# Kernel optimization log

Measured on AMD Instinct MI355X. Metric: run time of the kernel, lower is better.

## Reference

```python
import jax, jax.numpy as jnp
import numpy as np

ALPHA = 0.2

def _ema_last_weights(T, alpha, dtype):
    # Closed form for the final EMA value after the sequential recurrence:
    # ema_T = (1-a)^(T-1) * x_0 + sum_{t=1}^{T-1} a*(1-a)^(T-1-t) * x_t
    t = jnp.arange(T)
    w = alpha * (1.0 - alpha) ** (T - 1 - t)
    w = w.at[0].set((1.0 - alpha) ** (T - 1))
    return w.astype(dtype)


def setup_inputs() -> dict:
    key = jax.random.key(0)
    k1, k2 = jax.random.split(key)
    B, T, F = 64, 2048, 256
    x = jax.random.normal(k1, (B, T, F), dtype=jnp.float32)
    W = jax.random.normal(k2, (F, F), dtype=jnp.float32) * (1.0 / np.sqrt(F))
    b = jnp.zeros((F,), dtype=jnp.float32)
    return {"x": x, "W": W, "b": b}


def reference(x, W, b):
    B, T, F = x.shape
    # final-step EMA over time (equivalent to the sequential python loop)
    w = _ema_last_weights(T, ALPHA, x.dtype)          # [T]
    last_ref = jnp.einsum('t,btf->bf', w, x)[:, None, :]  # [B,1,F]
    # base residual predictor: per-timestep linear
    res = jnp.einsum('btf,fg->btg', x, W) + b          # [B,T,F]
    return last_ref + res
```

## Files before the change

### kernel.cpp

```cpp
#include <hip/hip_runtime.h>

#define Bdim 64
#define Tdim 2048
#define Fdim 256
#define TAIL 256
#define NCH 8
#define CHT 32

#define BM 64
#define BK 32
#define NCHUNK 8

typedef __bf16 bf16x8 __attribute__((ext_vector_type(8)));
typedef float f32x16 __attribute__((ext_vector_type(16)));
typedef unsigned short u16x8 __attribute__((ext_vector_type(8)));

__device__ __forceinline__ unsigned short bf16_rne(float f) {
  unsigned int u = __float_as_uint(f);
  u += 0x7FFFu + ((u >> 16) & 1u);
  return (unsigned short)(u >> 16);
}

__global__ void prep(const float* __restrict__ x, const float* __restrict__ W,
                     unsigned short* __restrict__ Wt, float* __restrict__ part) {
  int blk = blockIdx.x;
  if (blk < Fdim) {
    int i = blk * 256 + threadIdx.x;
    int g = i >> 8, f = i & 255;
    Wt[i] = bf16_rne(W[f * Fdim + g]);
  } else {
    int j = blk - Fdim;
    int b = j & 63, c = j >> 6;
    int f = threadIdx.x;
    int t0 = Tdim - TAIL + c * CHT;
    float w = 0.2f * exp2f((float)(Tdim - 1 - t0) * -0.32192809488736235f);
    const float* xp = x + ((size_t)b * Tdim + t0) * Fdim + f;
    float s = 0.f;
#pragma unroll
    for (int q = 0; q < CHT; ++q) {
      s += w * xp[(size_t)q * Fdim];
      w *= 1.25f;
    }
    part[(c * Bdim + b) * Fdim + f] = s;
  }
}

__global__ __launch_bounds__(256, 3)
void gemm_fused(const float* __restrict__ x, const unsigned short* __restrict__ Wt,
                const float* __restrict__ bias, const float* __restrict__ part,
                float* __restrict__ out) {
  __shared__ unsigned short Abuf[2][BM * BK];
  __shared__ unsigned short Bbuf[2][Fdim * BK];
  __shared__ float lref[Fdim];

  const int tid = threadIdx.x;
  const int blk = blockIdx.x;
  const int b = blk >> 5;
  const size_t row0 = (size_t)blk * BM;

  const int wave = tid >> 6;
  const int lane = tid & 63;
  const int lm = lane & 31;
  const int half = lane >> 5;

  {
    float s = bias[tid];
#pragma unroll
    for (int c = 0; c < NCH; ++c) s += part[(c * Bdim + b) * Fdim + tid];
    lref[tid] = s;
  }

  const int ar = tid >> 2;
  const int ag = tid & 3;
  const int aoff = ar * BK + ((ag ^ (ar & 3)) << 3);
  const float* asrc = x + (row0 + ar) * Fdim + ag * 8;

  const int bn = tid >> 2;
  const int bg = tid & 3;
  const unsigned short* bsrc = Wt + (size_t)bn * Fdim + bg * 8;
  const int boff = bn * BK + ((bg ^ (bn & 3)) << 3);

  f32x16 acc[2][2] = {};
  float4 Ar[2][2];
  u16x8 br0, br1, br2, br3;

  Ar[0][0] = *(const float4*)(asrc);
  Ar[0][1] = *(const float4*)(asrc + 4);
  br0 = *(const u16x8*)(bsrc + 0 * 64 * Fdim);
  br1 = *(const u16x8*)(bsrc + 1 * 64 * Fdim);
  br2 = *(const u16x8*)(bsrc + 2 * 64 * Fdim);
  br3 = *(const u16x8*)(bsrc + 3 * 64 * Fdim);
  {
    float4 v0 = Ar[0][0], v1 = Ar[0][1];
    u16x8 w;
    w[0] = bf16_rne(v0.x); w[1] = bf16_rne(v0.y);
    w[2] = bf16_rne(v0.z); w[3] = bf16_rne(v0.w);
    w[4] = bf16_rne(v1.x); w[5] = bf16_rne(v1.y);
    w[6] = bf16_rne(v1.z); w[7] = bf16_rne(v1.w);
    *(u16x8*)&Abuf[0][aoff] = w;
  }
  *(u16x8*)&Bbuf[0][boff + 0 * 64 * BK] = br0;
  *(u16x8*)&Bbuf[0][boff + 1 * 64 * BK] = br1;
  *(u16x8*)&Bbuf[0][boff + 2 * 64 * BK] = br2;
  *(u16x8*)&Bbuf[0][boff + 3 * 64 * BK] = br3;
  Ar[1][0] = *(const float4*)(asrc + BK);
  Ar[1][1] = *(const float4*)(asrc + BK + 4);
  __syncthreads();

#pragma unroll
  for (int c = 0; c < NCHUNK; ++c) {
    const int cur = c & 1, nxt = cur ^ 1;
    if (c + 2 < NCHUNK) {
      const float* s4 = asrc + (c + 2) * BK;
      Ar[cur][0] = *(const float4*)(s4);
      Ar[cur][1] = *(const float4*)(s4 + 4);
    }
    if (c + 1 < NCHUNK) {
      const unsigned short* bs = bsrc + (c + 1) * BK;
      br0 = *(const u16x8*)(bs + 0 * 64 * Fdim);
      br1 = *(const u16x8*)(bs + 1 * 64 * Fdim);
      br2 = *(const u16x8*)(bs + 2 * 64 * Fdim);
      br3 = *(const u16x8*)(bs + 3 * 64 * Fdim);
    }
#pragma unroll
    for (int s = 0; s < 2; ++s) {
      const int G = 2 * s + half;
      const int sw = ((G ^ (lm & 3)) << 3);
      bf16x8 a0 = *(const bf16x8*)&Abuf[cur][lm * BK + sw];
      bf16x8 a1 = *(const bf16x8*)&Abuf[cur][(32 + lm) * BK + sw];
      bf16x8 b0 = *(const bf16x8*)&Bbuf[cur][(wave * 64 + lm) * BK + sw];
      bf16x8 b1 = *(const bf16x8*)&Bbuf[cur][(wave * 64 + 32 + lm) * BK + sw];
      acc[0][0] = __builtin_amdgcn_mfma_f32_32x32x16_bf16(a0, b0, acc[0][0], 0, 0, 0);
      acc[0][1] = __builtin_amdgcn_mfma_f32_32x32x16_bf16(a0, b1, acc[0][1], 0, 0, 0);
      acc[1][0] = __builtin_amdgcn_mfma_f32_32x32x16_bf16(a1, b0, acc[1][0], 0, 0, 0);
      acc[1][1] = __builtin_amdgcn_mfma_f32_32x32x16_bf16(a1, b1, acc[1][1], 0, 0, 0);
    }
    if (c + 1 < NCHUNK) {
      float4 v0 = Ar[nxt][0], v1 = Ar[nxt][1];
      u16x8 w;
      w[0] = bf16_rne(v0.x); w[1] = bf16_rne(v0.y);
      w[2] = bf16_rne(v0.z); w[3] = bf16_rne(v0.w);
      w[4] = bf16_rne(v1.x); w[5] = bf16_rne(v1.y);
      w[6] = bf16_rne(v1.z); w[7] = bf16_rne(v1.w);
      *(u16x8*)&Abuf[nxt][aoff] = w;
      *(u16x8*)&Bbuf[nxt][boff + 0 * 64 * BK] = br0;
      *(u16x8*)&Bbuf[nxt][boff + 1 * 64 * BK] = br1;
      *(u16x8*)&Bbuf[nxt][boff + 2 * 64 * BK] = br2;
      *(u16x8*)&Bbuf[nxt][boff + 3 * 64 * BK] = br3;
      __syncthreads();
    }
  }

  float* op = out + row0 * Fdim;
  const int rbase = 4 * half;
#pragma unroll
  for (int i = 0; i < 2; ++i) {
#pragma unroll
    for (int j = 0; j < 2; ++j) {
      int n = wave * 64 + j * 32 + lm;
      float lb = lref[n];
#pragma unroll
      for (int r = 0; r < 16; ++r) {
        int rowi = i * 32 + (r & 3) + 8 * (r >> 2) + rbase;
        op[(size_t)rowi * Fdim + n] = acc[i][j][r] + lb;
      }
    }
  }
}

extern "C" void kernel_launch(void* const* d_in, const int* in_sizes, int n_in,
                              void* d_out, int out_size, void* d_ws, size_t ws_size,
                              hipStream_t stream) {
  const float* x = (const float*)d_in[0];
  const float* W = (const float*)d_in[1];
  const float* bias = (const float*)d_in[2];
  float* out = (float*)d_out;

  unsigned short* Wt = (unsigned short*)d_ws;
  float* part = (float*)((char*)d_ws + Fdim * Fdim * sizeof(unsigned short));

  prep<<<Fdim + Bdim * NCH, 256, 0, stream>>>(x, W, Wt, part);
  gemm_fused<<<(Bdim * Tdim) / BM, 256, 0, stream>>>(x, Wt, bias, part, out);
}
```

Baseline: 252.4 us.

## Pre-swizzle W into MFMA fragment order and load B directly to registers

The prep kernel now writes W in bf16 laid out in the exact per-lane MFMA operand order. The GEMM can then load B fragments straight from global memory into registers, which drops the B shared-memory buffer and its stores and reads. The A tile is also stored in fragment order, so LDS reads become simple lane-linear loads with no swizzle. The smaller LDS footprint lets launch bounds rise to 4 blocks per CU. In exchange, every wave re-reads its B fragments from global or L2, with more register pressure.

```diff
diff --git a/kernel.cpp b/kernel.cpp
--- a/kernel.cpp
+++ b/kernel.cpp
@@ -22,12 +22,15 @@
 }
 
 __global__ void prep(const float* __restrict__ x, const float* __restrict__ W,
-                     unsigned short* __restrict__ Wt, float* __restrict__ part) {
+                     unsigned short* __restrict__ Wf, float* __restrict__ part) {
   int blk = blockIdx.x;
   if (blk < Fdim) {
-    int i = blk * 256 + threadIdx.x;
-    int g = i >> 8, f = i & 255;
-    Wt[i] = bf16_rne(W[f * Fdim + g]);
+    int o = blk * 256 + threadIdx.x;
+    int e = o & 7, lane = (o >> 3) & 63, wh = (o >> 9) & 1, s = (o >> 10) & 1;
+    int c = (o >> 11) & 7, w = o >> 14;
+    int n = w * 64 + wh * 32 + (lane & 31);
+    int k = c * 32 + (2 * s + (lane >> 5)) * 8 + e;
+    Wf[o] = bf16_rne(W[k * Fdim + n]);
   } else {
     int j = blk - Fdim;
     int b = j & 63, c = j >> 6;
@@ -45,12 +48,11 @@
   }
 }
 
-__global__ __launch_bounds__(256, 3)
-void gemm_fused(const float* __restrict__ x, const unsigned short* __restrict__ Wt,
+__global__ __launch_bounds__(256, 4)
+void gemm_fused(const float* __restrict__ x, const unsigned short* __restrict__ Wf,
                 const float* __restrict__ bias, const float* __restrict__ part,
                 float* __restrict__ out) {
-  __shared__ unsigned short Abuf[2][BM * BK];
-  __shared__ unsigned short Bbuf[2][Fdim * BK];
+  __shared__ unsigned short Abuf[2][4 * 64 * 8];
   __shared__ float lref[Fdim];
 
   const int tid = threadIdx.x;
@@ -70,26 +72,23 @@
     lref[tid] = s;
   }
 
-  const int ar = tid >> 2;
-  const int ag = tid & 3;
-  const int aoff = ar * BK + ((ag ^ (ar & 3)) << 3);
-  const float* asrc = x + (row0 + ar) * Fdim + ag * 8;
+  const int srow = (wave >> 1) * 32 + lm;
+  const int scol = ((wave & 1) * 2 + half) * 8;
+  const float* asrc = x + (row0 + srow) * Fdim + scol;
+  const int adst = tid * 8;
 
-  const int bn = tid >> 2;
-  const int bg = tid & 3;
-  const unsigned short* bsrc = Wt + (size_t)bn * Fdim + bg * 8;
-  const int boff = bn * BK + ((bg ^ (bn & 3)) << 3);
+  const unsigned short* bsrc = Wf + (size_t)wave * (32 * 512) + lane * 8;
 
   f32x16 acc[2][2] = {};
   float4 Ar[2][2];
-  u16x8 br0, br1, br2, br3;
+  bf16x8 Bf[2][2];
 
-  Ar[0][0] = *(const float4*)(asrc);
+  Ar[0][0] = *(const float4*)asrc;
   Ar[0][1] = *(const float4*)(asrc + 4);
-  br0 = *(const u16x8*)(bsrc + 0 * 64 * Fdim);
-  br1 = *(const u16x8*)(bsrc + 1 * 64 * Fdim);
-  br2 = *(const u16x8*)(bsrc + 2 * 64 * Fdim);
-  br3 = *(const u16x8*)(bsrc + 3 * 64 * Fdim);
+  Bf[0][0] = *(const bf16x8*)(bsrc + 0 * 512);
+  Bf[0][1] = *(const bf16x8*)(bsrc + 1 * 512);
+  Bf[1][0] = *(const bf16x8*)(bsrc + 2 * 512);
+  Bf[1][1] = *(const bf16x8*)(bsrc + 3 * 512);
   {
     float4 v0 = Ar[0][0], v1 = Ar[0][1];
     u16x8 w;
@@ -97,12 +96,8 @@
     w[2] = bf16_rne(v0.z); w[3] = bf16_rne(v0.w);
     w[4] = bf16_rne(v1.x); w[5] = bf16_rne(v1.y);
     w[6] = bf16_rne(v1.z); w[7] = bf16_rne(v1.w);
-    *(u16x8*)&Abuf[0][aoff] = w;
+    *(u16x8*)&Abuf[0][adst] = w;
   }
-  *(u16x8*)&Bbuf[0][boff + 0 * 64 * BK] = br0;
-  *(u16x8*)&Bbuf[0][boff + 1 * 64 * BK] = br1;
-  *(u16x8*)&Bbuf[0][boff + 2 * 64 * BK] = br2;
-  *(u16x8*)&Bbuf[0][boff + 3 * 64 * BK] = br3;
   Ar[1][0] = *(const float4*)(asrc + BK);
   Ar[1][1] = *(const float4*)(asrc + BK + 4);
   __syncthreads();
@@ -112,28 +107,22 @@
     const int cur = c & 1, nxt = cur ^ 1;
     if (c + 2 < NCHUNK) {
       const float* s4 = asrc + (c + 2) * BK;
-      Ar[cur][0] = *(const float4*)(s4);
+      Ar[cur][0] = *(const float4*)s4;
       Ar[cur][1] = *(const float4*)(s4 + 4);
-    }
-    if (c + 1 < NCHUNK) {
-      const unsigned short* bs = bsrc + (c + 1) * BK;
-      br0 = *(const u16x8*)(bs + 0 * 64 * Fdim);
-      br1 = *(const u16x8*)(bs + 1 * 64 * Fdim);
-      br2 = *(const u16x8*)(bs + 2 * 64 * Fdim);
-      br3 = *(const u16x8*)(bs + 3 * 64 * Fdim);
     }
 #pragma unroll
     for (int s = 0; s < 2; ++s) {
-      const int G = 2 * s + half;
-      const int sw = ((G ^ (lm & 3)) << 3);
-      bf16x8 a0 = *(const bf16x8*)&Abuf[cur][lm * BK + sw];
-      bf16x8 a1 = *(const bf16x8*)&Abuf[cur][(32 + lm) * BK + sw];
-      bf16x8 b0 = *(const bf16x8*)&Bbuf[cur][(wave * 64 + lm) * BK + sw];
-      bf16x8 b1 = *(const bf16x8*)&Bbuf[cur][(wave * 64 + 32 + lm) * BK + sw];
-      acc[0][0] = __builtin_amdgcn_mfma_f32_32x32x16_bf16(a0, b0, acc[0][0], 0, 0, 0);
-      acc[0][1] = __builtin_amdgcn_mfma_f32_32x32x16_bf16(a0, b1, acc[0][1], 0, 0, 0);
-      acc[1][0] = __builtin_amdgcn_mfma_f32_32x32x16_bf16(a1, b0, acc[1][0], 0, 0, 0);
-      acc[1][1] = __builtin_amdgcn_mfma_f32_32x32x16_bf16(a1, b1, acc[1][1], 0, 0, 0);
+      bf16x8 a0 = *(const bf16x8*)&Abuf[cur][(s * 64 + lane) * 8];
+      bf16x8 a1 = *(const bf16x8*)&Abuf[cur][((2 + s) * 64 + lane) * 8];
+      acc[0][0] = __builtin_amdgcn_mfma_f32_32x32x16_bf16(a0, Bf[s][0], acc[0][0], 0, 0, 0);
+      acc[0][1] = __builtin_amdgcn_mfma_f32_32x32x16_bf16(a0, Bf[s][1], acc[0][1], 0, 0, 0);
+      acc[1][0] = __builtin_amdgcn_mfma_f32_32x32x16_bf16(a1, Bf[s][0], acc[1][0], 0, 0, 0);
+      acc[1][1] = __builtin_amdgcn_mfma_f32_32x32x16_bf16(a1, Bf[s][1], acc[1][1], 0, 0, 0);
+      if (c + 1 < NCHUNK) {
+        const unsigned short* bs = bsrc + (c + 1) * (4 * 512) + s * 1024;
+        Bf[s][0] = *(const bf16x8*)bs;
+        Bf[s][1] = *(const bf16x8*)(bs + 512);
+      }
     }
     if (c + 1 < NCHUNK) {
       float4 v0 = Ar[nxt][0], v1 = Ar[nxt][1];
@@ -142,11 +131,7 @@
       w[2] = bf16_rne(v0.z); w[3] = bf16_rne(v0.w);
       w[4] = bf16_rne(v1.x); w[5] = bf16_rne(v1.y);
       w[6] = bf16_rne(v1.z); w[7] = bf16_rne(v1.w);
-      *(u16x8*)&Abuf[nxt][aoff] = w;
-      *(u16x8*)&Bbuf[nxt][boff + 0 * 64 * BK] = br0;
-      *(u16x8*)&Bbuf[nxt][boff + 1 * 64 * BK] = br1;
-      *(u16x8*)&Bbuf[nxt][boff + 2 * 64 * BK] = br2;
-      *(u16x8*)&Bbuf[nxt][boff + 3 * 64 * BK] = br3;
+      *(u16x8*)&Abuf[nxt][adst] = w;
       __syncthreads();
     }
   }
@@ -176,9 +161,9 @@
   const float* bias = (const float*)d_in[2];
   float* out = (float*)d_out;
 
-  unsigned short* Wt = (unsigned short*)d_ws;
+  unsigned short* Wf = (unsigned short*)d_ws;
   float* part = (float*)((char*)d_ws + Fdim * Fdim * sizeof(unsigned short));
 
-  prep<<<Fdim + Bdim * NCH, 256, 0, stream>>>(x, W, Wt, part);
-  gemm_fused<<<(Bdim * Tdim) / BM, 256, 0, stream>>>(x, Wt, bias, part, out);
+  prep<<<Fdim + Bdim * NCH, 256, 0, stream>>>(x, W, Wf, part);
+  gemm_fused<<<(Bdim * Tdim) / BM, 256, 0, stream>>>(x, Wf, bias, part, out);
 }
```

Result: faster. 247.0 us (-2.1%).
